# Kernel optimization log

Hardware: AMD Instinct MI355X
Metric: run time of the kernel (lower is better)

The kernel has to match this reference:

```python
import jax, jax.numpy as jnp
import numpy as np

BN_EPS = 1e-5
K_HOPS = 10


def setup_inputs() -> dict:
    key = jax.random.key(0)
    ks = jax.random.split(key, 8)
    N, F, H, C, E = 169343, 128, 256, 40, 1200000
    return {
        "x": jax.random.normal(ks[0], (N, F), dtype=jnp.float32),
        "edge_index": jax.random.randint(ks[1], (2, E), 0, N, dtype=jnp.int64),
        "norm": jax.random.uniform(ks[2], (E,), dtype=jnp.float32),
        "W1": jax.random.normal(ks[3], (F, H), dtype=jnp.float32) * (1.0 / np.sqrt(F)),
        "b1": jnp.zeros((H,), jnp.float32),
        "bn_gamma": jnp.ones((H,), jnp.float32),
        "bn_beta": jnp.zeros((H,), jnp.float32),
        "bn_mean": jnp.zeros((H,), jnp.float32),
        "bn_var": jnp.ones((H,), jnp.float32),
        "W2": jax.random.normal(ks[4], (H, C), dtype=jnp.float32) * (1.0 / np.sqrt(H)),
        "b2": jnp.zeros((C,), jnp.float32),
        "proj_w": jax.random.normal(ks[5], (C,), dtype=jnp.float32) * (1.0 / np.sqrt(C)),
        "proj_b": jnp.zeros((1,), jnp.float32),
    }


def reference(x, edge_index, norm, W1, b1, bn_gamma, bn_beta, bn_mean, bn_var,
              W2, b2, proj_w, proj_b):
    N = x.shape[0]
    src, dst = edge_index[0], edge_index[1]

    # MLP head: Linear -> BatchNorm (eval, running stats) -> ReLU -> Linear
    h = x @ W1 + b1
    h = (h - bn_mean) * jax.lax.rsqrt(bn_var + BN_EPS) * bn_gamma + bn_beta
    h = jax.nn.relu(h)  # dropout: identity at inference
    h = h @ W2 + b2  # [N, C]

    # K-hop norm-weighted scatter-add propagation, collecting snapshots
    def hop(carry, _):
        msgs = norm[:, None] * carry[src]              # [E, C]
        nxt = jax.ops.segment_sum(msgs, dst, num_segments=N)
        return nxt, nxt

    _, hops = jax.lax.scan(hop, h, None, length=K_HOPS)  # [K, N, C]
    pps = jnp.concatenate([h[None], hops], axis=0)       # [K+1, N, C]
    pps = jnp.transpose(pps, (1, 0, 2))                  # [N, K+1, C]

    # sigmoid attention over hops, weighted combine
    retain = jax.nn.sigmoid(pps @ proj_w + proj_b[0])    # [N, K+1]
    out = jnp.einsum("nk,nkc->nc", retain, pps)          # [N, C]
    return jax.nn.log_softmax(out, axis=1)
```

## Files before the change

### kernel.cpp

```cpp
#include <hip/hip_runtime.h>
#include <hip/hip_bf16.h>
#include <math.h>

#define F 128
#define H 256
#define C 40
#define KHOPS 10
#define TM 32

typedef short bf16x8 __attribute__((ext_vector_type(8)));
typedef float f32x4 __attribute__((ext_vector_type(4)));

__device__ __forceinline__ void split3(float v, ushort& s1, ushort& s2, ushort& s3) {
    unsigned u = __float_as_uint(v);
    float f1 = __uint_as_float(u & 0xFFFF0000u);
    s1 = (ushort)(u >> 16);
    float r = v - f1;
    unsigned ur = __float_as_uint(r);
    float f2 = __uint_as_float(ur & 0xFFFF0000u);
    s2 = (ushort)(ur >> 16);
    float r2 = r - f2;
    s3 = (ushort)(__float_as_uint(r2) >> 16);
}

__global__ void k_count(const int* __restrict__ dst, int E, int* __restrict__ cnt) {
    int e = blockIdx.x * 256 + threadIdx.x;
    if (e < E) atomicAdd(&cnt[dst[e]], 1);
}

__global__ void k_scan1(const int* __restrict__ cnt, int n, int* __restrict__ bsum) {
    __shared__ int sh[256];
    int t = threadIdx.x;
    int base = blockIdx.x * 4096 + t * 16;
    int s = 0;
    for (int i = 0; i < 16; i++) { int idx = base + i; if (idx < n) s += cnt[idx]; }
    sh[t] = s; __syncthreads();
    for (int o = 128; o > 0; o >>= 1) {
        if (t < o) sh[t] += sh[t + o];
        __syncthreads();
    }
    if (t == 0) bsum[blockIdx.x] = sh[0];
}

__global__ void k_scan2(int* __restrict__ bsum, int nb) {
    if (threadIdx.x == 0) {
        int acc = 0;
        for (int i = 0; i < nb; i++) { int v = bsum[i]; bsum[i] = acc; acc += v; }
    }
}

__global__ void k_scan3(const int* __restrict__ cnt, int n, const int* __restrict__ bsum,
                        int* __restrict__ rp) {
    __shared__ int sh[256];
    int t = threadIdx.x;
    int base = blockIdx.x * 4096 + t * 16;
    int local[16]; int s = 0;
    for (int i = 0; i < 16; i++) {
        int idx = base + i;
        int v = (idx < n) ? cnt[idx] : 0;
        local[i] = v; s += v;
    }
    sh[t] = s; __syncthreads();
    for (int o = 1; o < 256; o <<= 1) {
        int v = (t >= o) ? sh[t - o] : 0;
        __syncthreads();
        sh[t] += v;
        __syncthreads();
    }
    int excl = (t == 0) ? 0 : sh[t - 1];
    int run = bsum[blockIdx.x] + excl;
    for (int i = 0; i < 16; i++) {
        int idx = base + i;
        if (idx < n) { rp[idx] = run; run += local[i]; }
    }
}

__global__ void k_fill(const int* __restrict__ src, const int* __restrict__ dst,
                       const float* __restrict__ nrm, int E, const int* __restrict__ rp,
                       int* __restrict__ cur, int2* __restrict__ ep) {
    int e = blockIdx.x * 256 + threadIdx.x;
    if (e < E) {
        int d = dst[e];
        int p = rp[d] + atomicAdd(&cur[d], 1);
        ep[p] = make_int2(src[e], __float_as_int(nrm[e]));
    }
}

__global__ void k_wsplit(const float* __restrict__ W1, ushort* __restrict__ w1a,
                         ushort* __restrict__ w1b, ushort* __restrict__ w1c) {
    int t = blockIdx.x * 256 + threadIdx.x;
    if (t < F * H) {
        int h = t / F, f = t % F;
        ushort a, b, c;
        split3(W1[(size_t)f * H + h], a, b, c);
        w1a[t] = a; w1b[t] = b; w1c[t] = c;
    }
}

__launch_bounds__(256)
__global__ void k_mlp(const float* __restrict__ x,
                      const ushort* __restrict__ w1a, const ushort* __restrict__ w1b,
                      const ushort* __restrict__ w1c,
                      const float* __restrict__ b1, const float* __restrict__ g,
                      const float* __restrict__ be, const float* __restrict__ mu,
                      const float* __restrict__ var, const float* __restrict__ W2,
                      const float* __restrict__ b2, const float* __restrict__ pw,
                      const float* __restrict__ pb,
                      float* __restrict__ hbuf, float* __restrict__ oacc, int N) {
    __shared__ ushort xsA[TM][136];
    __shared__ ushort xsB[TM][136];
    __shared__ ushort xsC[TM][136];
    __shared__ float h1s[TM][260];
    __shared__ float w2s[C][68];
    __shared__ float ascS[H], dscS[H];
    __shared__ float redc[256];
    __shared__ float sigv[TM];

    int t = threadIdx.x;
    int n0 = blockIdx.x * TM;

    for (int kk = 0; kk < 4; kk++) {
        int idx = kk * 256 + t;
        int node = idx >> 5, f4 = idx & 31;
        int n = n0 + node;
        float4 v = (n < N) ? ((const float4*)x)[(size_t)n * (F / 4) + f4]
                           : make_float4(0.f, 0.f, 0.f, 0.f);
        ushort4 pa, pm, pc;
        split3(v.x, pa.x, pm.x, pc.x);
        split3(v.y, pa.y, pm.y, pc.y);
        split3(v.z, pa.z, pm.z, pc.z);
        split3(v.w, pa.w, pm.w, pc.w);
        *((ushort4*)&xsA[node][f4 * 4]) = pa;
        *((ushort4*)&xsB[node][f4 * 4]) = pm;
        *((ushort4*)&xsC[node][f4 * 4]) = pc;
    }
    {
        float a = g[t] * rsqrtf(var[t] + 1e-5f);
        ascS[t] = a;
        dscS[t] = (b1[t] - mu[t]) * a + be[t];
    }
    __syncthreads();

    int lane = t & 63, wv = t >> 6, quad = lane >> 4, lq = lane & 15;
    int n0w = wv * 64;
    f32x4 acc[2][4];
    #pragma unroll
    for (int mi = 0; mi < 2; mi++)
        #pragma unroll
        for (int ni = 0; ni < 4; ni++)
            acc[mi][ni] = (f32x4){0.f, 0.f, 0.f, 0.f};

    #pragma unroll
    for (int ks = 0; ks < 4; ks++) {
        int k0 = ks * 32 + quad * 8;
        bf16x8 a1[2], a2[2], a3[2];
        #pragma unroll
        for (int mi = 0; mi < 2; mi++) {
            int row = mi * 16 + lq;
            a1[mi] = *((const bf16x8*)&xsA[row][k0]);
            a2[mi] = *((const bf16x8*)&xsB[row][k0]);
            a3[mi] = *((const bf16x8*)&xsC[row][k0]);
        }
        #pragma unroll
        for (int ni = 0; ni < 4; ni++) {
            size_t wo = (size_t)(n0w + ni * 16 + lq) * F + k0;
            bf16x8 q1 = *((const bf16x8*)(w1a + wo));
            bf16x8 q2 = *((const bf16x8*)(w1b + wo));
            bf16x8 q3 = *((const bf16x8*)(w1c + wo));
            #pragma unroll
            for (int mi = 0; mi < 2; mi++) {
                acc[mi][ni] = __builtin_amdgcn_mfma_f32_16x16x32_bf16(a1[mi], q1, acc[mi][ni], 0, 0, 0);
                acc[mi][ni] = __builtin_amdgcn_mfma_f32_16x16x32_bf16(a1[mi], q2, acc[mi][ni], 0, 0, 0);
                acc[mi][ni] = __builtin_amdgcn_mfma_f32_16x16x32_bf16(a2[mi], q1, acc[mi][ni], 0, 0, 0);
                acc[mi][ni] = __builtin_amdgcn_mfma_f32_16x16x32_bf16(a1[mi], q3, acc[mi][ni], 0, 0, 0);
                acc[mi][ni] = __builtin_amdgcn_mfma_f32_16x16x32_bf16(a2[mi], q2, acc[mi][ni], 0, 0, 0);
                acc[mi][ni] = __builtin_amdgcn_mfma_f32_16x16x32_bf16(a3[mi], q1, acc[mi][ni], 0, 0, 0);
            }
        }
    }

    #pragma unroll
    for (int ni = 0; ni < 4; ni++) {
        int h = n0w + ni * 16 + lq;
        float a = ascS[h], d = dscS[h];
        #pragma unroll
        for (int mi = 0; mi < 2; mi++) {
            #pragma unroll
            for (int r = 0; r < 4; r++) {
                int node = mi * 16 + quad * 4 + r;
                float v = acc[mi][ni][r] * a + d;
                h1s[node][h] = v > 0.f ? v : 0.f;
            }
        }
    }
    __syncthreads();

    int n_loc = t >> 3, cg = t & 7;
    float acc2[5];
    #pragma unroll
    for (int j = 0; j < 5; j++) acc2[j] = b2[cg * 5 + j];

    for (int h0 = 0; h0 < H; h0 += 64) {
        for (int kk = 0; kk < 10; kk++) {
            int idx = kk * 256 + t;
            if (idx < 2560) {
                int hh = idx / 40, c = idx % 40;
                w2s[c][hh] = W2[(size_t)(h0 + hh) * C + c];
            }
        }
        __syncthreads();
        #pragma unroll 4
        for (int hh = 0; hh < 64; hh += 4) {
            float4 hv = *((const float4*)&h1s[n_loc][h0 + hh]);
            #pragma unroll
            for (int j = 0; j < 5; j++) {
                float4 w4 = *((const float4*)&w2s[cg * 5 + j][hh]);
                acc2[j] += hv.x * w4.x + hv.y * w4.y + hv.z * w4.z + hv.w * w4.w;
            }
        }
        __syncthreads();
    }

    #pragma unroll
    for (int j = 0; j < 5; j++) h1s[n_loc][cg * 5 + j] = acc2[j];
    float part = 0.f;
    #pragma unroll
    for (int j = 0; j < 5; j++) part += acc2[j] * pw[cg * 5 + j];
    redc[t] = part;
    __syncthreads();
    if (cg == 0) {
        float s = 0.f;
        #pragma unroll
        for (int q = 0; q < 8; q++) s += redc[n_loc * 8 + q];
        sigv[n_loc] = 1.f / (1.f + expf(-(s + pb[0])));
    }
    __syncthreads();
    if (t < 160) {
        int row = t / 5, p = t % 5;
        int n = n0 + row;
        if (n < N) {
            float4 a, b;
            a.x = h1s[row][8 * p + 0]; a.y = h1s[row][8 * p + 1];
            a.z = h1s[row][8 * p + 2]; a.w = h1s[row][8 * p + 3];
            b.x = h1s[row][8 * p + 4]; b.y = h1s[row][8 * p + 5];
            b.z = h1s[row][8 * p + 6]; b.w = h1s[row][8 * p + 7];
            float4* hp = (float4*)(hbuf + (size_t)n * C + 8 * p);
            hp[0] = a; hp[1] = b;
            float sg = sigv[row];
            float4 oa, ob;
            oa.x = sg * a.x; oa.y = sg * a.y; oa.z = sg * a.z; oa.w = sg * a.w;
            ob.x = sg * b.x; ob.y = sg * b.y; ob.z = sg * b.z; ob.w = sg * b.w;
            float4* op = (float4*)(oacc + (size_t)n * C + 8 * p);
            op[0] = oa; op[1] = ob;
        }
    }
}

__global__ void k_hop(const float4* __restrict__ cur4, float4* __restrict__ nxt4,
                      float4* __restrict__ oacc4, const int* __restrict__ rp,
                      const int2* __restrict__ ep,
                      const float* __restrict__ pw, const float* __restrict__ pb, int N) {
    __shared__ float red[320];
    __shared__ float sig[64];
    int t = threadIdx.x;
    int nl = t / 5, p = t % 5;
    int n = blockIdx.x * 64 + nl;
    int c0 = 2 * p;
    float4 a0 = make_float4(0.f, 0.f, 0.f, 0.f);
    float4 a1 = make_float4(0.f, 0.f, 0.f, 0.f);
    if (n < N) {
        int b = rp[n], e = rp[n + 1];
        int j = b;
        for (; j + 4 <= e; j += 4) {
            int2 e0 = ep[j], e1 = ep[j + 1], e2 = ep[j + 2], e3 = ep[j + 3];
            const float4* r0 = cur4 + (size_t)e0.x * 10 + c0;
            const float4* r1 = cur4 + (size_t)e1.x * 10 + c0;
            const float4* r2 = cur4 + (size_t)e2.x * 10 + c0;
            const float4* r3 = cur4 + (size_t)e3.x * 10 + c0;
            float4 v00 = r0[0], v01 = r0[1];
            float4 v10 = r1[0], v11 = r1[1];
            float4 v20 = r2[0], v21 = r2[1];
            float4 v30 = r3[0], v31 = r3[1];
            float w0 = __int_as_float(e0.y), w1 = __int_as_float(e1.y);
            float w2 = __int_as_float(e2.y), w3 = __int_as_float(e3.y);
            a0.x += w0 * v00.x; a0.y += w0 * v00.y; a0.z += w0 * v00.z; a0.w += w0 * v00.w;
            a1.x += w0 * v01.x; a1.y += w0 * v01.y; a1.z += w0 * v01.z; a1.w += w0 * v01.w;
            a0.x += w1 * v10.x; a0.y += w1 * v10.y; a0.z += w1 * v10.z; a0.w += w1 * v10.w;
            a1.x += w1 * v11.x; a1.y += w1 * v11.y; a1.z += w1 * v11.z; a1.w += w1 * v11.w;
            a0.x += w2 * v20.x; a0.y += w2 * v20.y; a0.z += w2 * v20.z; a0.w += w2 * v20.w;
            a1.x += w2 * v21.x; a1.y += w2 * v21.y; a1.z += w2 * v21.z; a1.w += w2 * v21.w;
            a0.x += w3 * v30.x; a0.y += w3 * v30.y; a0.z += w3 * v30.z; a0.w += w3 * v30.w;
            a1.x += w3 * v31.x; a1.y += w3 * v31.y; a1.z += w3 * v31.z; a1.w += w3 * v31.w;
        }
        if (j + 2 <= e) {
            int2 e0 = ep[j], e1 = ep[j + 1];
            const float4* r0 = cur4 + (size_t)e0.x * 10 + c0;
            const float4* r1 = cur4 + (size_t)e1.x * 10 + c0;
            float4 v00 = r0[0], v01 = r0[1];
            float4 v10 = r1[0], v11 = r1[1];
            float w0 = __int_as_float(e0.y), w1 = __int_as_float(e1.y);
            a0.x += w0 * v00.x; a0.y += w0 * v00.y; a0.z += w0 * v00.z; a0.w += w0 * v00.w;
            a1.x += w0 * v01.x; a1.y += w0 * v01.y; a1.z += w0 * v01.z; a1.w += w0 * v01.w;
            a0.x += w1 * v10.x; a0.y += w1 * v10.y; a0.z += w1 * v10.z; a0.w += w1 * v10.w;
            a1.x += w1 * v11.x; a1.y += w1 * v11.y; a1.z += w1 * v11.z; a1.w += w1 * v11.w;
            j += 2;
        }
        if (j < e) {
            int2 e0 = ep[j];
            const float4* r0 = cur4 + (size_t)e0.x * 10 + c0;
            float4 v00 = r0[0], v01 = r0[1];
            float w0 = __int_as_float(e0.y);
            a0.x += w0 * v00.x; a0.y += w0 * v00.y; a0.z += w0 * v00.z; a0.w += w0 * v00.w;
            a1.x += w0 * v01.x; a1.y += w0 * v01.y; a1.z += w0 * v01.z; a1.w += w0 * v01.w;
        }
        nxt4[(size_t)n * 10 + c0] = a0;
        nxt4[(size_t)n * 10 + c0 + 1] = a1;
    }
    float4 pw0 = ((const float4*)pw)[c0];
    float4 pw1 = ((const float4*)pw)[c0 + 1];
    red[t] = a0.x * pw0.x + a0.y * pw0.y + a0.z * pw0.z + a0.w * pw0.w
           + a1.x * pw1.x + a1.y * pw1.y + a1.z * pw1.z + a1.w * pw1.w;
    __syncthreads();
    if (p == 0) {
        float s = red[t] + red[t + 1] + red[t + 2] + red[t + 3] + red[t + 4];
        sig[nl] = 1.f / (1.f + expf(-(s + pb[0])));
    }
    __syncthreads();
    if (n < N) {
        float sg = sig[nl];
        size_t o = (size_t)n * 10 + c0;
        float4 v0 = oacc4[o], v1 = oacc4[o + 1];
        v0.x += sg * a0.x; v0.y += sg * a0.y; v0.z += sg * a0.z; v0.w += sg * a0.w;
        v1.x += sg * a1.x; v1.y += sg * a1.y; v1.z += sg * a1.z; v1.w += sg * a1.w;
        oacc4[o] = v0;
        oacc4[o + 1] = v1;
    }
}

__global__ void k_lsm(float4* __restrict__ io, int N) {
    __shared__ float red[320];
    __shared__ float statm[32];
    __shared__ float stats[32];
    int t = threadIdx.x;
    int nl = t / 10, c4 = t % 10;
    int n = blockIdx.x * 32 + nl;
    bool ok = n < N;
    float4 v = ok ? io[(size_t)n * 10 + c4] : make_float4(-1e30f, -1e30f, -1e30f, -1e30f);
    red[t] = fmaxf(fmaxf(v.x, v.y), fmaxf(v.z, v.w));
    __syncthreads();
    if (c4 == 0) {
        float m = -1e30f;
        #pragma unroll
        for (int q = 0; q < 10; q++) m = fmaxf(m, red[nl * 10 + q]);
        statm[nl] = m;
    }
    __syncthreads();
    float m = statm[nl];
    float e0 = expf(v.x - m), e1 = expf(v.y - m), e2 = expf(v.z - m), e3 = expf(v.w - m);
    red[t] = e0 + e1 + e2 + e3;
    __syncthreads();
    if (c4 == 0) {
        float s = 0.f;
        #pragma unroll
        for (int q = 0; q < 10; q++) s += red[nl * 10 + q];
        stats[nl] = logf(s);
    }
    __syncthreads();
    if (ok) {
        float ls = stats[nl];
        io[(size_t)n * 10 + c4] = make_float4(v.x - m - ls, v.y - m - ls, v.z - m - ls, v.w - m - ls);
    }
}

extern "C" void kernel_launch(void* const* d_in, const int* in_sizes, int n_in,
                              void* d_out, int out_size, void* d_ws, size_t ws_size,
                              hipStream_t stream) {
    const float* x   = (const float*)d_in[0];
    const int*   ei  = (const int*)d_in[1];
    const float* nrm = (const float*)d_in[2];
    const float* W1  = (const float*)d_in[3];
    const float* b1  = (const float*)d_in[4];
    const float* g   = (const float*)d_in[5];
    const float* be  = (const float*)d_in[6];
    const float* mu  = (const float*)d_in[7];
    const float* var = (const float*)d_in[8];
    const float* W2  = (const float*)d_in[9];
    const float* b2  = (const float*)d_in[10];
    const float* pw  = (const float*)d_in[11];
    const float* pb  = (const float*)d_in[12];
    float* out = (float*)d_out;

    int N = in_sizes[0] / F;
    int E = in_sizes[2];

    char* w = (char*)d_ws;
    auto alloc = [&](size_t bytes) {
        void* p = (void*)w;
        w += ((bytes + 255) / 256) * 256;
        return p;
    };
    int*    rp     = (int*)alloc((size_t)(N + 1) * 4);
    int*    cursor = (int*)alloc((size_t)(N + 1) * 4);
    int*    bsum   = (int*)alloc(1024);
    int2*   ep     = (int2*)alloc((size_t)E * 8);
    ushort* w1a    = (ushort*)alloc((size_t)F * H * 2);
    ushort* w1b    = (ushort*)alloc((size_t)F * H * 2);
    ushort* w1c    = (ushort*)alloc((size_t)F * H * 2);
    float*  bufA   = (float*)alloc((size_t)N * C * 4);
    float*  bufB   = (float*)alloc((size_t)N * C * 4);

    hipMemsetAsync(cursor, 0, (size_t)(N + 1) * 4, stream);

    k_count<<<(E + 255) / 256, 256, 0, stream>>>(ei + E, E, cursor);

    int n1 = N + 1;
    int NB = (n1 + 4095) / 4096;
    k_scan1<<<NB, 256, 0, stream>>>(cursor, n1, bsum);
    k_scan2<<<1, 64, 0, stream>>>(bsum, NB);
    k_scan3<<<NB, 256, 0, stream>>>(cursor, n1, bsum, rp);

    hipMemsetAsync(cursor, 0, (size_t)(N + 1) * 4, stream);
    k_fill<<<(E + 255) / 256, 256, 0, stream>>>(ei, ei + E, nrm, E, rp, cursor, ep);

    k_wsplit<<<(F * H + 255) / 256, 256, 0, stream>>>(W1, w1a, w1b, w1c);

    k_mlp<<<(N + TM - 1) / TM, 256, 0, stream>>>(x, w1a, w1b, w1c, b1, g, be, mu, var,
                                                 W2, b2, pw, pb, bufA, out, N);

    int nodeBlocks64 = (N + 63) / 64;
    float* cur = bufA;
    float* nxt = bufB;
    for (int k = 0; k < KHOPS; k++) {
        k_hop<<<nodeBlocks64, 320, 0, stream>>>((const float4*)cur, (float4*)nxt, (float4*)out,
                                                rp, ep, pw, pb, N);
        float* tmp = cur; cur = nxt; nxt = tmp;
    }

    int nodeBlocks32 = (N + 31) / 32;
    k_lsm<<<nodeBlocks32, 320, 0, stream>>>((float4*)out, N);
}
```

Measured before the change: 1.049 ms.

## Fuse log-softmax into last hop and cut MLP shared memory for occupancy

The log-softmax kernel is folded into the final propagation hop, which also skips writing the unused next-hop buffer and the intermediate accumulator. This removes one launch and a full read/write pass over the output. The MLP kernel now keeps x in LDS as fp32 and splits it into three bf16 parts at fragment-load time. It also reuses the x buffer for the W2 tile and the partial sums, splits the second GEMM across two halves of the block, and adds a 3-blocks-per-SM launch bound. The aim is less LDS per block and higher occupancy, at the cost of repeating the split arithmetic inside the MFMA loop.

```diff
diff --git a/kernel.cpp b/kernel.cpp
--- a/kernel.cpp
+++ b/kernel.cpp
@@ -97,7 +97,7 @@
     }
 }
 
-__launch_bounds__(256)
+__launch_bounds__(256, 3)
 __global__ void k_mlp(const float* __restrict__ x,
                       const ushort* __restrict__ w1a, const ushort* __restrict__ w1b,
                       const ushort* __restrict__ w1c,
@@ -107,13 +107,9 @@
                       const float* __restrict__ b2, const float* __restrict__ pw,
                       const float* __restrict__ pb,
                       float* __restrict__ hbuf, float* __restrict__ oacc, int N) {
-    __shared__ ushort xsA[TM][136];
-    __shared__ ushort xsB[TM][136];
-    __shared__ ushort xsC[TM][136];
+    __shared__ float xs[TM][132];
     __shared__ float h1s[TM][260];
-    __shared__ float w2s[C][68];
     __shared__ float ascS[H], dscS[H];
-    __shared__ float redc[256];
     __shared__ float sigv[TM];
 
     int t = threadIdx.x;
@@ -125,14 +121,7 @@
         int n = n0 + node;
         float4 v = (n < N) ? ((const float4*)x)[(size_t)n * (F / 4) + f4]
                            : make_float4(0.f, 0.f, 0.f, 0.f);
-        ushort4 pa, pm, pc;
-        split3(v.x, pa.x, pm.x, pc.x);
-        split3(v.y, pa.y, pm.y, pc.y);
-        split3(v.z, pa.z, pm.z, pc.z);
-        split3(v.w, pa.w, pm.w, pc.w);
-        *((ushort4*)&xsA[node][f4 * 4]) = pa;
-        *((ushort4*)&xsB[node][f4 * 4]) = pm;
-        *((ushort4*)&xsC[node][f4 * 4]) = pc;
+        *((float4*)&xs[node][f4 * 4]) = v;
     }
     {
         float a = g[t] * rsqrtf(var[t] + 1e-5f);
@@ -157,9 +146,15 @@
         #pragma unroll
         for (int mi = 0; mi < 2; mi++) {
             int row = mi * 16 + lq;
-            a1[mi] = *((const bf16x8*)&xsA[row][k0]);
-            a2[mi] = *((const bf16x8*)&xsB[row][k0]);
-            a3[mi] = *((const bf16x8*)&xsC[row][k0]);
+            float4 f0 = *((const float4*)&xs[row][k0]);
+            float4 f1 = *((const float4*)&xs[row][k0 + 4]);
+            float fv[8] = {f0.x, f0.y, f0.z, f0.w, f1.x, f1.y, f1.z, f1.w};
+            #pragma unroll
+            for (int e = 0; e < 8; e++) {
+                ushort sa, sb, sc;
+                split3(fv[e], sa, sb, sc);
+                a1[mi][e] = (short)sa; a2[mi][e] = (short)sb; a3[mi][e] = (short)sc;
+            }
         }
         #pragma unroll
         for (int ni = 0; ni < 4; ni++) {
@@ -195,46 +190,77 @@
     }
     __syncthreads();
 
-    int n_loc = t >> 3, cg = t & 7;
-    float acc2[5];
+    int kh = t >> 7;
+    int u  = t & 127;
+    int ng = u >> 3;
+    int cg = u & 7;
+    float acc2[2][5];
     #pragma unroll
-    for (int j = 0; j < 5; j++) acc2[j] = b2[cg * 5 + j];
-
-    for (int h0 = 0; h0 < H; h0 += 64) {
+    for (int j = 0; j < 5; j++) { acc2[0][j] = 0.f; acc2[1][j] = 0.f; }
+
+    float (*w2s)[68] = (float (*)[68])&xs[0][0];
+
+    for (int ch = 0; ch < 4; ch++) {
         for (int kk = 0; kk < 10; kk++) {
             int idx = kk * 256 + t;
             if (idx < 2560) {
                 int hh = idx / 40, c = idx % 40;
-                w2s[c][hh] = W2[(size_t)(h0 + hh) * C + c];
+                w2s[c][hh] = W2[(size_t)(ch * 64 + hh) * C + c];
             }
         }
         __syncthreads();
-        #pragma unroll 4
-        for (int hh = 0; hh < 64; hh += 4) {
-            float4 hv = *((const float4*)&h1s[n_loc][h0 + hh]);
-            #pragma unroll
-            for (int j = 0; j < 5; j++) {
-                float4 w4 = *((const float4*)&w2s[cg * 5 + j][hh]);
-                acc2[j] += hv.x * w4.x + hv.y * w4.y + hv.z * w4.z + hv.w * w4.w;
+        if ((ch >> 1) == kh) {
+            int hb = ch * 64;
+            #pragma unroll 2
+            for (int hh = 0; hh < 64; hh += 4) {
+                float4 ha = *((const float4*)&h1s[ng][hb + hh]);
+                float4 hc = *((const float4*)&h1s[ng + 16][hb + hh]);
+                #pragma unroll
+                for (int j = 0; j < 5; j++) {
+                    float4 w4 = *((const float4*)&w2s[cg * 5 + j][hh]);
+                    acc2[0][j] += ha.x * w4.x + ha.y * w4.y + ha.z * w4.z + ha.w * w4.w;
+                    acc2[1][j] += hc.x * w4.x + hc.y * w4.y + hc.z * w4.z + hc.w * w4.w;
+                }
             }
         }
         __syncthreads();
     }
 
-    #pragma unroll
-    for (int j = 0; j < 5; j++) h1s[n_loc][cg * 5 + j] = acc2[j];
-    float part = 0.f;
-    #pragma unroll
-    for (int j = 0; j < 5; j++) part += acc2[j] * pw[cg * 5 + j];
-    redc[t] = part;
-    __syncthreads();
-    if (cg == 0) {
-        float s = 0.f;
-        #pragma unroll
-        for (int q = 0; q < 8; q++) s += redc[n_loc * 8 + q];
-        sigv[n_loc] = 1.f / (1.f + expf(-(s + pb[0])));
-    }
-    __syncthreads();
+    float (*pbuf)[40] = (float (*)[40])&xs[0][0];
+    if (kh == 1) {
+        #pragma unroll
+        for (int j = 0; j < 5; j++) {
+            pbuf[ng][cg * 5 + j] = acc2[0][j];
+            pbuf[ng + 16][cg * 5 + j] = acc2[1][j];
+        }
+    }
+    __syncthreads();
+    if (kh == 0) {
+        float p0 = 0.f, p1 = 0.f;
+        #pragma unroll
+        for (int j = 0; j < 5; j++) {
+            int c = cg * 5 + j;
+            float bb = b2[c];
+            float h0 = acc2[0][j] + pbuf[ng][c] + bb;
+            float h1v = acc2[1][j] + pbuf[ng + 16][c] + bb;
+            float wv2 = pw[c];
+            p0 += h0 * wv2;
+            p1 += h1v * wv2;
+            h1s[ng][c] = h0;
+            h1s[ng + 16][c] = h1v;
+        }
+        #pragma unroll
+        for (int m = 1; m < 8; m <<= 1) {
+            p0 += __shfl_xor(p0, m);
+            p1 += __shfl_xor(p1, m);
+        }
+        if (cg == 0) {
+            sigv[ng]      = 1.f / (1.f + expf(-(p0 + pb[0])));
+            sigv[ng + 16] = 1.f / (1.f + expf(-(p1 + pb[0])));
+        }
+    }
+    __syncthreads();
+
     if (t < 160) {
         int row = t / 5, p = t % 5;
         int n = n0 + row;
@@ -259,9 +285,12 @@
 __global__ void k_hop(const float4* __restrict__ cur4, float4* __restrict__ nxt4,
                       float4* __restrict__ oacc4, const int* __restrict__ rp,
                       const int2* __restrict__ ep,
-                      const float* __restrict__ pw, const float* __restrict__ pb, int N) {
+                      const float* __restrict__ pw, const float* __restrict__ pb,
+                      int N, int last) {
     __shared__ float red[320];
     __shared__ float sig[64];
+    __shared__ float statm[64];
+    __shared__ float stats[64];
     int t = threadIdx.x;
     int nl = t / 5, p = t % 5;
     int n = blockIdx.x * 64 + nl;
@@ -313,8 +342,10 @@
             a0.x += w0 * v00.x; a0.y += w0 * v00.y; a0.z += w0 * v00.z; a0.w += w0 * v00.w;
             a1.x += w0 * v01.x; a1.y += w0 * v01.y; a1.z += w0 * v01.z; a1.w += w0 * v01.w;
         }
-        nxt4[(size_t)n * 10 + c0] = a0;
-        nxt4[(size_t)n * 10 + c0 + 1] = a1;
+        if (!last) {
+            nxt4[(size_t)n * 10 + c0] = a0;
+            nxt4[(size_t)n * 10 + c0 + 1] = a1;
+        }
     }
     float4 pw0 = ((const float4*)pw)[c0];
     float4 pw1 = ((const float4*)pw)[c0 + 1];
@@ -326,49 +357,49 @@
         sig[nl] = 1.f / (1.f + expf(-(s + pb[0])));
     }
     __syncthreads();
+    float4 v0 = make_float4(0.f, 0.f, 0.f, 0.f);
+    float4 v1 = make_float4(0.f, 0.f, 0.f, 0.f);
+    size_t o = (size_t)n * 10 + c0;
     if (n < N) {
         float sg = sig[nl];
-        size_t o = (size_t)n * 10 + c0;
-        float4 v0 = oacc4[o], v1 = oacc4[o + 1];
+        v0 = oacc4[o]; v1 = oacc4[o + 1];
         v0.x += sg * a0.x; v0.y += sg * a0.y; v0.z += sg * a0.z; v0.w += sg * a0.w;
         v1.x += sg * a1.x; v1.y += sg * a1.y; v1.z += sg * a1.z; v1.w += sg * a1.w;
-        oacc4[o] = v0;
-        oacc4[o + 1] = v1;
-    }
-}
-
-__global__ void k_lsm(float4* __restrict__ io, int N) {
-    __shared__ float red[320];
-    __shared__ float statm[32];
-    __shared__ float stats[32];
-    int t = threadIdx.x;
-    int nl = t / 10, c4 = t % 10;
-    int n = blockIdx.x * 32 + nl;
-    bool ok = n < N;
-    float4 v = ok ? io[(size_t)n * 10 + c4] : make_float4(-1e30f, -1e30f, -1e30f, -1e30f);
-    red[t] = fmaxf(fmaxf(v.x, v.y), fmaxf(v.z, v.w));
-    __syncthreads();
-    if (c4 == 0) {
-        float m = -1e30f;
-        #pragma unroll
-        for (int q = 0; q < 10; q++) m = fmaxf(m, red[nl * 10 + q]);
-        statm[nl] = m;
-    }
-    __syncthreads();
-    float m = statm[nl];
-    float e0 = expf(v.x - m), e1 = expf(v.y - m), e2 = expf(v.z - m), e3 = expf(v.w - m);
-    red[t] = e0 + e1 + e2 + e3;
-    __syncthreads();
-    if (c4 == 0) {
+        if (!last) {
+            oacc4[o] = v0;
+            oacc4[o + 1] = v1;
+        }
+    }
+    if (last) {
+        bool ok = n < N;
+        float mx = fmaxf(fmaxf(fmaxf(v0.x, v0.y), fmaxf(v0.z, v0.w)),
+                         fmaxf(fmaxf(v1.x, v1.y), fmaxf(v1.z, v1.w)));
+        red[t] = ok ? mx : -1e30f;
+        __syncthreads();
+        if (p == 0) {
+            float m = fmaxf(fmaxf(fmaxf(red[t], red[t + 1]), fmaxf(red[t + 2], red[t + 3])),
+                            red[t + 4]);
+            statm[nl] = m;
+        }
+        __syncthreads();
+        float m = statm[nl];
         float s = 0.f;
-        #pragma unroll
-        for (int q = 0; q < 10; q++) s += red[nl * 10 + q];
-        stats[nl] = logf(s);
-    }
-    __syncthreads();
-    if (ok) {
-        float ls = stats[nl];
-        io[(size_t)n * 10 + c4] = make_float4(v.x - m - ls, v.y - m - ls, v.z - m - ls, v.w - m - ls);
+        if (ok) {
+            s = expf(v0.x - m) + expf(v0.y - m) + expf(v0.z - m) + expf(v0.w - m)
+              + expf(v1.x - m) + expf(v1.y - m) + expf(v1.z - m) + expf(v1.w - m);
+        }
+        red[t] = s;
+        __syncthreads();
+        if (p == 0) {
+            float ssum = red[t] + red[t + 1] + red[t + 2] + red[t + 3] + red[t + 4];
+            stats[nl] = logf(ssum);
+        }
+        __syncthreads();
+        if (ok) {
+            float ls = statm[nl] + stats[nl];
+            oacc4[o]     = make_float4(v0.x - ls, v0.y - ls, v0.z - ls, v0.w - ls);
+            oacc4[o + 1] = make_float4(v1.x - ls, v1.y - ls, v1.z - ls, v1.w - ls);
+        }
     }
 }
 
@@ -432,10 +463,7 @@
     float* nxt = bufB;
     for (int k = 0; k < KHOPS; k++) {
         k_hop<<<nodeBlocks64, 320, 0, stream>>>((const float4*)cur, (float4*)nxt, (float4*)out,
-                                                rp, ep, pw, pb, N);
+                                                rp, ep, pw, pb, N, (k == KHOPS - 1) ? 1 : 0);
         float* tmp = cur; cur = nxt; nxt = tmp;
     }
-
-    int nodeBlocks32 = (N + 31) / 32;
-    k_lsm<<<nodeBlocks32, 320, 0, stream>>>((float4*)out, N);
-}
+}
```

After: 1.045 ms. About the same (-0.4%).
